# Kernel tuning notes

Measured on AMD Instinct MI355X. Metric: run time of the kernel, lower is better.

## Reference

```python
import jax, jax.numpy as jnp
import numpy as np

K = 5            # spline kernel size per dim
NUM_CLASSES = 10
EPS = 1e-4       # matches module's normalize eps
ROUTING_ITERS = 3
_BITS = jnp.array([[(b >> 2) & 1, (b >> 1) & 1, b & 1] for b in range(8)], dtype=jnp.float32)  # [8,3]


def normalize(t, axis=-1):
    return t / (jnp.sqrt(jnp.sum(t * t, axis=axis, keepdims=True)) + EPS)


def quat_mul(q, r):
    # quaternions stored (x, y, z, w) -- module sets identity as [:,:,:,3]=1
    qx, qy, qz, qw = q[..., 0], q[..., 1], q[..., 2], q[..., 3]
    rx, ry, rz, rw = r[..., 0], r[..., 1], r[..., 2], r[..., 3]
    return jnp.stack([
        qw * rx + qx * rw + qy * rz - qz * ry,
        qw * ry - qx * rz + qy * rw + qz * rx,
        qw * rz + qx * ry - qy * rx + qz * rw,
        qw * rw - qx * rx - qy * ry - qz * rz,
    ], axis=-1)


def spline_conv(x, pseudo, src, dst, W, root, bias, n_nodes):
    # degree-1 open B-spline conv, kernel 5^3, in=1, out=16
    v = pseudo * (K - 1)                                   # [E,3]
    i0 = jnp.clip(jnp.floor(v), 0, K - 2)                  # [E,3]
    frac = v - i0
    i0 = i0.astype(jnp.int32)
    idx = i0[:, None, :] + _BITS.astype(jnp.int32)[None]   # [E,8,3]
    kflat = (idx[..., 0] * K + idx[..., 1]) * K + idx[..., 2]  # [E,8]
    wb = jnp.prod(jnp.where(_BITS[None] > 0, frac[:, None, :], 1.0 - frac[:, None, :]), axis=-1)  # [E,8]
    Wg = W[kflat]                                          # [E,8,16] irregular gather (dominant traffic)
    wk = jnp.einsum('eb,ebo->eo', wb, Wg)                  # [E,16]
    msg = x[src] * wk                                      # [E,16] (in-channels = 1)
    agg = jax.ops.segment_sum(msg, dst, num_segments=n_nodes)
    deg = jax.ops.segment_sum(jnp.ones_like(dst, dtype=x.dtype), dst, num_segments=n_nodes)
    return agg / jnp.maximum(deg, 1.0)[:, None] + x @ root + bias


def caps_layer(pose, act, q):
    # pose [N,I,4], act [N,I], q [I,J,4] -> pose [N,J,4], act [N,J]
    qn = normalize(q)
    pred = normalize(quat_mul(qn[None], pose[:, :, None, :]))  # [N,I,J,4]
    b = jnp.zeros(pred.shape[:3], dtype=pose.dtype)
    for _ in range(ROUTING_ITERS):
        c = jax.nn.softmax(b, axis=2) * act[:, :, None]
        s = jnp.einsum('nij,nijq->njq', c, pred)
        v = normalize(s)
        b = b + jnp.einsum('nijq,njq->nij', pred, v)
    act_out = jax.nn.sigmoid(jnp.einsum('nij,nijq,njq->nj', c, pred, v))
    return v, act_out


def pool_by_agreement(pose, act, pos, G, start, size):
    # voxel-grid clustering + agreement-weighted quaternion averaging
    g = jnp.clip(jnp.floor((pos - start) / size), 0, G - 1).astype(jnp.int32)  # [N,3]
    vid = (g[:, 0] * G + g[:, 1]) * G + g[:, 2]
    V = G ** 3
    s = jax.ops.segment_sum(act[:, :, None] * pose, vid, num_segments=V)  # [V,J,4]
    m = normalize(s)
    agree = jnp.sum(pose * m[vid], axis=-1)                                # [N,J]
    wsum = jax.ops.segment_sum(act, vid, num_segments=V)
    cnt = jax.ops.segment_sum(jnp.ones((pose.shape[0],), pose.dtype), vid, num_segments=V)
    act_out = jax.nn.sigmoid(jax.ops.segment_sum(act * agree, vid, num_segments=V) / (wsum + EPS))
    pos_out = jax.ops.segment_sum(pos, vid, num_segments=V) / (cnt[:, None] + EPS)
    return m, act_out, pos_out


def forward(x, pos, pseudo, W_spline, root, bias, lin_w, lin_b, q0, q1, q3, q5, q6, q7, edge_index):
    N = x.shape[0]
    src, dst = edge_index[0], edge_index[1]
    h = spline_conv(x, pseudo, src, dst, W_spline, root, bias, N)   # [N,16]
    quats = jax.nn.elu(h) @ lin_w + lin_b                           # [N,4]
    pose = normalize(quats.reshape(N, 1, 4))                        # [N,1,4]
    act = x.reshape(N, 1)                                           # expand to num_caps_in=1
    pose, act = caps_layer(pose, act, q0)                           # 1 -> 6
    pose, act = caps_layer(pose, act, q1)                           # 6 -> 6
    min_pos, max_pos = pos.min(), pos.max()
    rng = max_pos + 0.001 - min_pos
    pose, act, p = pool_by_agreement(pose, act, pos, 32, min_pos, rng / 32)   # -> 32768 voxels
    pose, act = caps_layer(pose, act, q3)                           # 6 -> 8
    pose, act, p = pool_by_agreement(pose, act, p, 8, min_pos, rng / 8)       # -> 512
    pose, act = caps_layer(pose, act, q5)                           # 8 -> 12
    pose, act, p = pool_by_agreement(pose, act, p, 2, min_pos, rng / 2)       # -> 8
    pose, act = caps_layer(pose, act, q6)                           # 12 -> 14
    pose, act, p = pool_by_agreement(pose, act, p, 1, min_pos - 0.5, max_pos - min_pos + 1.0)  # -> 1
    pose, act = caps_layer(pose, act, q7)                           # 14 -> 10
    return act                                                      # [1, 10]


def setup_inputs() -> dict:
    key = jax.random.key(0)
    ks = jax.random.split(key, 16)
    N, E = 50000, 800000
    def caps_q(k, i, j):
        return jax.random.normal(k, (i, j, 4), dtype=jnp.float32)
    return {
        'x': jax.random.uniform(ks[0], (N, 1), dtype=jnp.float32),
        'pos': jax.random.uniform(ks[1], (N, 3), dtype=jnp.float32),
        'pseudo': jax.random.uniform(ks[2], (E, 3), dtype=jnp.float32),
        'W_spline': jax.random.normal(ks[3], (K ** 3, 16), dtype=jnp.float32) * 0.1,
        'root': jax.random.normal(ks[4], (1, 16), dtype=jnp.float32) * 0.1,
        'bias': jnp.zeros((16,), dtype=jnp.float32),
        'lin_w': jax.random.normal(ks[5], (16, 4), dtype=jnp.float32) * 0.25,
        'lin_b': jnp.zeros((4,), dtype=jnp.float32),
        'q0': caps_q(ks[6], 1, 6),
        'q1': caps_q(ks[7], 6, 6),
        'q3': caps_q(ks[8], 6, 8),
        'q5': caps_q(ks[9], 8, 12),
        'q6': caps_q(ks[10], 12, 14),
        'q7': caps_q(ks[11], 14, NUM_CLASSES),
        'edge_index': jax.random.randint(ks[12], (2, E), 0, N, dtype=jnp.int32),
    }


def reference(x, pos, pseudo, W_spline, root, bias, lin_w, lin_b, q0, q1, q3, q5, q6, q7, edge_index):
    return forward(x, pos, pseudo, W_spline, root, bias, lin_w, lin_b, q0, q1, q3, q5, q6, q7, edge_index)
```

## Files before the change

kernel.cpp:

```cpp
#include <hip/hip_runtime.h>
#include <math.h>

#define EPS 1e-4f

__device__ __forceinline__ float sigmoidf_(float x){ return 1.0f/(1.0f+expf(-x)); }

__device__ __forceinline__ unsigned f2u_(float f){
    unsigned u = __float_as_uint(f);
    return (u & 0x80000000u) ? ~u : (u | 0x80000000u);
}
__device__ __forceinline__ float u2f_(unsigned u){
    unsigned b = (u & 0x80000000u) ? (u & 0x7FFFFFFFu) : ~u;
    return __uint_as_float(b);
}

__global__ void minmax_kernel(const float* __restrict__ p, int n, unsigned* mm){
    float lo = INFINITY, hi = -INFINITY;
    for (int i = blockIdx.x*blockDim.x + threadIdx.x; i < n; i += gridDim.x*blockDim.x){
        float v = p[i]; lo = fminf(lo, v); hi = fmaxf(hi, v);
    }
    for (int off = 32; off > 0; off >>= 1){
        lo = fminf(lo, __shfl_down(lo, off));
        hi = fmaxf(hi, __shfl_down(hi, off));
    }
    __shared__ float slo[8], shi[8];
    int wid = threadIdx.x >> 6;
    if ((threadIdx.x & 63) == 0){ slo[wid] = lo; shi[wid] = hi; }
    __syncthreads();
    if (threadIdx.x == 0){
        int nw = blockDim.x >> 6;
        for (int w = 1; w < nw; w++){ lo = fminf(lo, slo[w]); hi = fmaxf(hi, shi[w]); }
        atomicMin(&mm[0], f2u_(lo));
        atomicMax(&mm[1], f2u_(hi));
    }
}

struct __align__(32) Rec { float fr0, fr1, fr2, xv; int base, nxt, pad0, pad1; };

__global__ void edge_pack(const int* __restrict__ ei, const float* __restrict__ pseudo,
                          const float* __restrict__ x,
                          int* __restrict__ head, Rec* __restrict__ rec, int E, int N){
    int e = blockIdx.x*blockDim.x + threadIdx.x;
    if (e >= E) return;
    float p0 = pseudo[3*e], p1 = pseudo[3*e+1], p2 = pseudo[3*e+2];
    int s = ei[e], d = ei[E + e];
    float v0 = p0*4.f, v1 = p1*4.f, v2 = p2*4.f;
    float f0 = fminf(fmaxf(floorf(v0), 0.f), 3.f);
    float f1 = fminf(fmaxf(floorf(v1), 0.f), 3.f);
    float f2 = fminf(fmaxf(floorf(v2), 0.f), 3.f);
    float4 fv = make_float4(v0 - f0, v1 - f1, v2 - f2, x[s]);
    *reinterpret_cast<float4*>(&rec[e]) = fv;
    int base = ((int)f0*5 + (int)f1)*5 + (int)f2;
    int nx = atomicExch(&head[(e & 7)*N + d], e);
    *reinterpret_cast<int2*>(&rec[e].base) = make_int2(base, nx);
}

__device__ __forceinline__ int voxel_id(const float* __restrict__ pos, int n, int G,
                                        float start, float size){
    int g[3];
    #pragma unroll
    for (int k = 0; k < 3; k++){
        float gg = floorf((pos[(size_t)n*3 + k] - start) / size);
        gg = fminf(fmaxf(gg, 0.f), (float)(G - 1));
        g[k] = (int)gg;
    }
    return (g[0]*G + g[1])*G + g[2];
}

__device__ __forceinline__ void pool_geom(const unsigned* mm, int G, int mode,
                                          float& start, float& size){
    float mn = u2f_(mm[0]), mx = u2f_(mm[1]);
    if (mode == 0){ start = mn; size = (mx + 0.001f - mn) / (float)G; }
    else          { start = mn - 0.5f; size = mx - mn + 1.0f; }
}

__global__ void elist_node(const float* __restrict__ pos, int* __restrict__ head,
                           int* __restrict__ nxt, int N, int G, int mode,
                           const unsigned* __restrict__ mm){
    int n = blockIdx.x*blockDim.x + threadIdx.x;
    if (n >= N) return;
    float start, size; pool_geom(mm, G, mode, start, size);
    int v = voxel_id(pos, n, G, start, size);
    nxt[n] = atomicExch(&head[v], n);
}

__global__ __launch_bounds__(256)
void spline_node_kernel(const float* __restrict__ x, const Rec* __restrict__ rec,
                        const int* __restrict__ head,
                        const float* __restrict__ W,
                        const float* __restrict__ root, const float* __restrict__ bias,
                        const float* __restrict__ lin_w, const float* __restrict__ lin_b,
                        float* __restrict__ pose, float* __restrict__ act, int N){
    __shared__ float Ws[125*17];
    for (int i = threadIdx.x; i < 125*16; i += blockDim.x)
        Ws[(i >> 4)*17 + (i & 15)] = W[i];
    __syncthreads();
    int t = blockIdx.x*blockDim.x + threadIdx.x;
    int n = t >> 3;
    int k = t & 7;
    if (n >= N) return;

    float agg[16];
    #pragma unroll
    for (int o = 0; o < 16; o++) agg[o] = 0.f;

    int cnt = 0;
    for (int e = head[k*N + n]; e >= 0; ){
        const Rec* rp = &rec[e];
        float4 rv = *reinterpret_cast<const float4*>(rp);
        int2  ri = *reinterpret_cast<const int2*>(&rp->base);
        e = ri.y;
        float fr0 = rv.x, fr1 = rv.y, fr2 = rv.z, xv = rv.w;
        #pragma unroll
        for (int b = 0; b < 8; b++){
            int b0 = (b >> 2) & 1, b1 = (b >> 1) & 1, b2 = b & 1;
            float w = (b0 ? fr0 : 1.f - fr0) * (b1 ? fr1 : 1.f - fr1) * (b2 ? fr2 : 1.f - fr2);
            w *= xv;
            const float* Wr = &Ws[(ri.x + b0*25 + b1*5 + b2)*17];
            #pragma unroll
            for (int o = 0; o < 16; o++) agg[o] += w * Wr[o];
        }
        cnt++;
    }

    #pragma unroll
    for (int o = 0; o < 16; o++){
        agg[o] += __shfl_xor(agg[o], 1);
        agg[o] += __shfl_xor(agg[o], 2);
        agg[o] += __shfl_xor(agg[o], 4);
    }
    cnt += __shfl_xor(cnt, 1);
    cnt += __shfl_xor(cnt, 2);
    cnt += __shfl_xor(cnt, 4);

    if (k != 0) return;

    float deg = fmaxf((float)cnt, 1.0f);
    float xs = x[n];
    float qv0 = lin_b[0], qv1 = lin_b[1], qv2 = lin_b[2], qv3 = lin_b[3];
    #pragma unroll
    for (int o = 0; o < 16; o++){
        float h = agg[o] / deg + xs * root[o] + bias[o];
        float e = (h > 0.f) ? h : expm1f(h);
        qv0 += e * lin_w[o*4 + 0];
        qv1 += e * lin_w[o*4 + 1];
        qv2 += e * lin_w[o*4 + 2];
        qv3 += e * lin_w[o*4 + 3];
    }
    float inv = 1.0f / (sqrtf(qv0*qv0 + qv1*qv1 + qv2*qv2 + qv3*qv3) + EPS);
    pose[(size_t)n*4 + 0] = qv0*inv;
    pose[(size_t)n*4 + 1] = qv1*inv;
    pose[(size_t)n*4 + 2] = qv2*inv;
    pose[(size_t)n*4 + 3] = qv3*inv;
    act[n] = xs;
}

template<int I, int J, int NPB>
__global__ __launch_bounds__(NPB*I*J)
void caps_coop_kernel(const float* __restrict__ poseIn, const float* __restrict__ actIn,
                      const float* __restrict__ q, float* __restrict__ poseOut,
                      float* __restrict__ actOut, int N){
    const int IJ = I*J;
    const int tid = threadIdx.x;
    const int nl  = tid / IJ;
    const int li  = tid - nl*IJ;
    const int i   = li / J;
    const int j   = li - i*J;
    const int node = blockIdx.x*NPB + nl;
    const bool on = (node < N);

    __shared__ float redA[NPB][I*J];
    __shared__ float redB[NPB][I*J];
    __shared__ float cp[NPB][I*J*4];
    __shared__ float vsh[NPB][J*4];

    float prx=0.f, pry=0.f, prz=0.f, prw=0.f, ai=0.f;
    if (on){
        float qx = q[li*4+0], qy = q[li*4+1], qz = q[li*4+2], qw = q[li*4+3];
        float qinv = 1.0f/(sqrtf(qx*qx+qy*qy+qz*qz+qw*qw)+EPS);
        qx*=qinv; qy*=qinv; qz*=qinv; qw*=qinv;
        const float* pp = &poseIn[((size_t)node*I + i)*4];
        float rx=pp[0], ry=pp[1], rz=pp[2], rw=pp[3];
        ai = actIn[(size_t)node*I + i];
        float tx = qw*rx + qx*rw + qy*rz - qz*ry;
        float ty = qw*ry - qx*rz + qy*rw + qz*rx;
        float tz = qw*rz + qx*ry - qy*rx + qz*rw;
        float tw = qw*rw - qx*rx - qy*ry - qz*rz;
        float pinv = 1.0f/(sqrtf(tx*tx+ty*ty+tz*tz+tw*tw)+EPS);
        prx=tx*pinv; pry=ty*pinv; prz=tz*pinv; prw=tw*pinv;
    }

    float b = 0.f, c = 0.f;
    for (int t = 0; t < 3; t++){
        redA[nl][li] = b;
        __syncthreads();
        float mb = -INFINITY;
        #pragma unroll
        for (int jj = 0; jj < J; jj++) mb = fmaxf(mb, redA[nl][i*J+jj]);
        float e = expf(b - mb);
        redB[nl][li] = e;
        __syncthreads();
        float s = 0.f;
        #pragma unroll
        for (int jj = 0; jj < J; jj++) s += redB[nl][i*J+jj];
        c = ai * e / s;
        cp[nl][li*4+0] = c*prx; cp[nl][li*4+1] = c*pry;
        cp[nl][li*4+2] = c*prz; cp[nl][li*4+3] = c*prw;
        __syncthreads();
        for (int idx = li; idx < J*4; idx += IJ){
            int jj = idx >> 2, comp = idx & 3;
            float acc = 0.f;
            #pragma unroll
            for (int ii = 0; ii < I; ii++) acc += cp[nl][(ii*J+jj)*4+comp];
            vsh[nl][idx] = acc;
        }
        __syncthreads();
        if (li < J){
            float a0=vsh[nl][li*4], a1=vsh[nl][li*4+1], a2=vsh[nl][li*4+2], a3=vsh[nl][li*4+3];
            float inv = 1.0f/(sqrtf(a0*a0+a1*a1+a2*a2+a3*a3)+EPS);
            vsh[nl][li*4]=a0*inv; vsh[nl][li*4+1]=a1*inv;
            vsh[nl][li*4+2]=a2*inv; vsh[nl][li*4+3]=a3*inv;
        }
        __syncthreads();
        if (t < 2){
            b += prx*vsh[nl][j*4] + pry*vsh[nl][j*4+1] + prz*vsh[nl][j*4+2] + prw*vsh[nl][j*4+3];
            __syncthreads();
        } else {
            redA[nl][li] = c*(prx*vsh[nl][j*4] + pry*vsh[nl][j*4+1]
                            + prz*vsh[nl][j*4+2] + prw*vsh[nl][j*4+3]);
            __syncthreads();
            if (li < J && on){
                float acc = 0.f;
                #pragma unroll
                for (int ii = 0; ii < I; ii++) acc += redA[nl][ii*J+li];
                actOut[(size_t)node*J + li] = sigmoidf_(acc);
                poseOut[((size_t)node*J+li)*4+0] = vsh[nl][li*4+0];
                poseOut[((size_t)node*J+li)*4+1] = vsh[nl][li*4+1];
                poseOut[((size_t)node*J+li)*4+2] = vsh[nl][li*4+2];
                poseOut[((size_t)node*J+li)*4+3] = vsh[nl][li*4+3];
            }
        }
    }
}

template<int J>
__global__ __launch_bounds__(256)
void pool1_gather_kernel(const float* __restrict__ pose, const float* __restrict__ act,
                         const float* __restrict__ pos,
                         const int* __restrict__ head, const int* __restrict__ nxt,
                         float* __restrict__ poseOut, float* __restrict__ actOut,
                         float* __restrict__ posOut, int V){
    int v = blockIdx.x*blockDim.x + threadIdx.x;
    if (v >= V) return;

    float s[J][4], w[J], ps0=0.f, ps1=0.f, ps2=0.f;
    #pragma unroll
    for (int j = 0; j < J; j++){ s[j][0]=0.f; s[j][1]=0.f; s[j][2]=0.f; s[j][3]=0.f; w[j]=0.f; }

    int cnt = 0;
    for (int n = head[v]; n >= 0; n = nxt[n]){
        const float* pb = &pose[(size_t)n*J*4];
        const float* ab = &act[(size_t)n*J];
        #pragma unroll
        for (int j = 0; j < J; j++){
            float aj = ab[j];
            s[j][0] += aj*pb[j*4+0];
            s[j][1] += aj*pb[j*4+1];
            s[j][2] += aj*pb[j*4+2];
            s[j][3] += aj*pb[j*4+3];
            w[j] += aj;
        }
        ps0 += pos[(size_t)n*3+0];
        ps1 += pos[(size_t)n*3+1];
        ps2 += pos[(size_t)n*3+2];
        cnt++;
    }
    #pragma unroll
    for (int j = 0; j < J; j++){
        float inv = 1.0f/(sqrtf(s[j][0]*s[j][0]+s[j][1]*s[j][1]+
                                s[j][2]*s[j][2]+s[j][3]*s[j][3])+EPS);
        s[j][0]*=inv; s[j][1]*=inv; s[j][2]*=inv; s[j][3]*=inv;
    }
    float ag[J];
    #pragma unroll
    for (int j = 0; j < J; j++) ag[j] = 0.f;
    for (int n = head[v]; n >= 0; n = nxt[n]){
        const float* pb = &pose[(size_t)n*J*4];
        const float* ab = &act[(size_t)n*J];
        #pragma unroll
        for (int j = 0; j < J; j++){
            float agree = pb[j*4+0]*s[j][0] + pb[j*4+1]*s[j][1]
                        + pb[j*4+2]*s[j][2] + pb[j*4+3]*s[j][3];
            ag[j] += ab[j]*agree;
        }
    }
    #pragma unroll
    for (int j = 0; j < J; j++){
        size_t o = (size_t)v*J + j;
        actOut[o] = sigmoidf_(ag[j] / (w[j] + EPS));
        poseOut[o*4+0] = s[j][0];
        poseOut[o*4+1] = s[j][1];
        poseOut[o*4+2] = s[j][2];
        poseOut[o*4+3] = s[j][3];
    }
    float c = (float)cnt + EPS;
    posOut[(size_t)v*3+0] = ps0 / c;
    posOut[(size_t)v*3+1] = ps1 / c;
    posOut[(size_t)v*3+2] = ps2 / c;
}

template<int V, int J, int CH, int NCHUNK>
__global__ void pool_priv1(const float4* __restrict__ poseIn, const float* __restrict__ actIn,
                           const float* __restrict__ posIn,
                           float* __restrict__ s, float* __restrict__ wsum,
                           float* __restrict__ cnt, float* __restrict__ psum,
                           int N, int G, int mode, const unsigned* __restrict__ mm){
    __shared__ float s_[V*CH*4];
    __shared__ float wsum_[V*CH];
    __shared__ float cnt_[V];
    __shared__ float psum_[V*3];
    const int chunk = blockIdx.x % NCHUNK;
    const int slice = blockIdx.x / NCHUNK;
    const int nslices = gridDim.x / NCHUNK;
    const int c0 = chunk * CH;

    for (int t = threadIdx.x; t < V*CH*4; t += blockDim.x) s_[t] = 0.f;
    for (int t = threadIdx.x; t < V*CH; t += blockDim.x) wsum_[t] = 0.f;
    if (chunk == 0){
        for (int t = threadIdx.x; t < V; t += blockDim.x) cnt_[t] = 0.f;
        for (int t = threadIdx.x; t < V*3; t += blockDim.x) psum_[t] = 0.f;
    }
    __syncthreads();

    float start, size; pool_geom(mm, G, mode, start, size);
    int per = (N + nslices - 1) / nslices;
    int n0 = slice * per, n1 = min(N, n0 + per);

    for (int n = n0 + (int)threadIdx.x; n < n1; n += blockDim.x){
        int vid = voxel_id(posIn, n, G, start, size);
        #pragma unroll
        for (int jj = 0; jj < CH; jj++){
            int j = c0 + jj;
            float aj = actIn[(size_t)n*J + j];
            float4 p = poseIn[(size_t)n*J + j];
            int b = (vid*CH + jj)*4;
            atomicAdd(&s_[b+0], aj*p.x);
            atomicAdd(&s_[b+1], aj*p.y);
            atomicAdd(&s_[b+2], aj*p.z);
            atomicAdd(&s_[b+3], aj*p.w);
            atomicAdd(&wsum_[vid*CH + jj], aj);
        }
        if (chunk == 0){
            atomicAdd(&cnt_[vid], 1.0f);
            atomicAdd(&psum_[vid*3+0], posIn[(size_t)n*3+0]);
            atomicAdd(&psum_[vid*3+1], posIn[(size_t)n*3+1]);
            atomicAdd(&psum_[vid*3+2], posIn[(size_t)n*3+2]);
        }
    }
    __syncthreads();

    for (int t = threadIdx.x; t < V*CH*4; t += blockDim.x){
        float val = s_[t];
        if (val != 0.f){
            int v = t / (CH*4), r = t % (CH*4);
            atomicAdd(&s[((size_t)v*J + c0)*4 + r], val);
        }
    }
    for (int t = threadIdx.x; t < V*CH; t += blockDim.x){
        float val = wsum_[t];
        if (val != 0.f){
            int v = t / CH, jj = t % CH;
            atomicAdd(&wsum[(size_t)v*J + c0 + jj], val);
        }
    }
    if (chunk == 0){
        for (int t = threadIdx.x; t < V; t += blockDim.x)
            if (cnt_[t] != 0.f) atomicAdd(&cnt[t], cnt_[t]);
        for (int t = threadIdx.x; t < V*3; t += blockDim.x)
            if (psum_[t] != 0.f) atomicAdd(&psum[t], psum_[t]);
    }
}

template<int V, int J>
__global__ void pool_priv2(const float4* __restrict__ poseIn, const float* __restrict__ actIn,
                           const float* __restrict__ posIn, const float4* __restrict__ m,
                           float* __restrict__ agacc,
                           int N, int G, int mode, const unsigned* __restrict__ mm){
    __shared__ float ag_[V*J];
    for (int t = threadIdx.x; t < V*J; t += blockDim.x) ag_[t] = 0.f;
    __syncthreads();
    float start, size; pool_geom(mm, G, mode, start, size);
    int nslices = gridDim.x;
    int per = (N + nslices - 1) / nslices;
    int n0 = blockIdx.x * per, n1 = min(N, n0 + per);
    for (int n = n0 + (int)threadIdx.x; n < n1; n += blockDim.x){
        int vid = voxel_id(posIn, n, G, start, size);
        #pragma unroll
        for (int j = 0; j < J; j++){
            float4 p  = poseIn[(size_t)n*J + j];
            float4 mv = m[(size_t)vid*J + j];
            float agree = p.x*mv.x + p.y*mv.y + p.z*mv.z + p.w*mv.w;
            atomicAdd(&ag_[vid*J + j], actIn[(size_t)n*J + j]*agree);
        }
    }
    __syncthreads();
    for (int t = threadIdx.x; t < V*J; t += blockDim.x)
        if (ag_[t] != 0.f) atomicAdd(&agacc[t], ag_[t]);
}

__global__ void pool_m(const float* __restrict__ s, float* __restrict__ m, int VJ){
    int t = blockIdx.x*blockDim.x + threadIdx.x;
    if (t >= VJ) return;
    float a = s[(size_t)t*4], b = s[(size_t)t*4+1], c = s[(size_t)t*4+2], d = s[(size_t)t*4+3];
    float inv = 1.0f / (sqrtf(a*a + b*b + c*c + d*d) + EPS);
    m[(size_t)t*4]   = a*inv;
    m[(size_t)t*4+1] = b*inv;
    m[(size_t)t*4+2] = c*inv;
    m[(size_t)t*4+3] = d*inv;
}

__global__ void pool_fin(const float* __restrict__ agacc, const float* __restrict__ wsum,
                         const float* __restrict__ cnt, const float* __restrict__ psum,
                         float* __restrict__ actOut, float* __restrict__ posOut, int V, int J){
    int t = blockIdx.x*blockDim.x + threadIdx.x;
    if (t >= V*J) return;
    int v = t / J, j = t % J;
    actOut[t] = sigmoidf_(agacc[t] / (wsum[t] + EPS));
    if (j == 0){
        float c = cnt[v] + EPS;
        posOut[(size_t)v*3 + 0] = psum[(size_t)v*3 + 0] / c;
        posOut[(size_t)v*3 + 1] = psum[(size_t)v*3 + 1] / c;
        posOut[(size_t)v*3 + 2] = psum[(size_t)v*3 + 2] / c;
    }
}

template<int V, int J, int CH>
__global__ void pool_fused_kernel(const float* __restrict__ poseIn, const float* __restrict__ actIn,
                                  const float* __restrict__ posIn,
                                  float* __restrict__ poseOut, float* __restrict__ actOut,
                                  float* __restrict__ posOut,
                                  int N, int G, int mode, const unsigned* __restrict__ mm){
    __shared__ float s_[V*CH*4];
    __shared__ float wsum_[V*CH];
    __shared__ float ag_[V*CH];
    __shared__ float cnt_[V];
    __shared__ float psum_[V*3];
    const int c0 = blockIdx.x * CH;

    for (int t = threadIdx.x; t < V*CH*4; t += blockDim.x) s_[t] = 0.f;
    for (int t = threadIdx.x; t < V*CH; t += blockDim.x){ wsum_[t] = 0.f; ag_[t] = 0.f; }
    if (blockIdx.x == 0){
        for (int t = threadIdx.x; t < V; t += blockDim.x) cnt_[t] = 0.f;
        for (int t = threadIdx.x; t < V*3; t += blockDim.x) psum_[t] = 0.f;
    }
    __syncthreads();

    float start, size; pool_geom(mm, G, mode, start, size);

    for (int n = threadIdx.x; n < N; n += blockDim.x){
        int vid = voxel_id(posIn, n, G, start, size);
        #pragma unroll
        for (int jj = 0; jj < CH; jj++){
            int j = c0 + jj;
            float aj = actIn[(size_t)n*J + j];
            const float* pb = &poseIn[((size_t)n*J + j)*4];
            int b = (vid*CH + jj)*4;
            atomicAdd(&s_[b+0], aj*pb[0]);
            atomicAdd(&s_[b+1], aj*pb[1]);
            atomicAdd(&s_[b+2], aj*pb[2]);
            atomicAdd(&s_[b+3], aj*pb[3]);
            atomicAdd(&wsum_[vid*CH + jj], aj);
        }
        if (blockIdx.x == 0){
            atomicAdd(&cnt_[vid], 1.0f);
            atomicAdd(&psum_[vid*3+0], posIn[(size_t)n*3+0]);
            atomicAdd(&psum_[vid*3+1], posIn[(size_t)n*3+1]);
            atomicAdd(&psum_[vid*3+2], posIn[(size_t)n*3+2]);
        }
    }
    __syncthreads();

    for (int t = threadIdx.x; t < V*CH; t += blockDim.x){
        float a = s_[t*4], b = s_[t*4+1], c = s_[t*4+2], d = s_[t*4+3];
        float inv = 1.0f / (sqrtf(a*a + b*b + c*c + d*d) + EPS);
        s_[t*4] = a*inv; s_[t*4+1] = b*inv; s_[t*4+2] = c*inv; s_[t*4+3] = d*inv;
    }
    __syncthreads();

    for (int n = threadIdx.x; n < N; n += blockDim.x){
        int vid = voxel_id(posIn, n, G, start, size);
        #pragma unroll
        for (int jj = 0; jj < CH; jj++){
            int j = c0 + jj;
            const float* pb = &poseIn[((size_t)n*J + j)*4];
            const float* mb = &s_[(vid*CH + jj)*4];
            float agree = pb[0]*mb[0] + pb[1]*mb[1] + pb[2]*mb[2] + pb[3]*mb[3];
            atomicAdd(&ag_[vid*CH + jj], actIn[(size_t)n*J + j]*agree);
        }
    }
    __syncthreads();

    for (int t = threadIdx.x; t < V*CH; t += blockDim.x){
        int v = t / CH, jj = t % CH;
        size_t o = (size_t)v*J + c0 + jj;
        actOut[o] = sigmoidf_(ag_[t] / (wsum_[t] + EPS));
        poseOut[o*4+0] = s_[t*4+0];
        poseOut[o*4+1] = s_[t*4+1];
        poseOut[o*4+2] = s_[t*4+2];
        poseOut[o*4+3] = s_[t*4+3];
    }
    if (blockIdx.x == 0){
        for (int v = threadIdx.x; v < V; v += blockDim.x){
            float c = cnt_[v] + EPS;
            posOut[(size_t)v*3+0] = psum_[(size_t)v*3+0] / c;
            posOut[(size_t)v*3+1] = psum_[(size_t)v*3+1] / c;
            posOut[(size_t)v*3+2] = psum_[(size_t)v*3+2] / c;
        }
    }
}

extern "C" void kernel_launch(void* const* d_in, const int* in_sizes, int n_in,
                              void* d_out, int out_size, void* d_ws, size_t ws_size,
                              hipStream_t stream){
    const float* x      = (const float*)d_in[0];
    const float* pos    = (const float*)d_in[1];
    const float* pseudo = (const float*)d_in[2];
    const float* Wsp    = (const float*)d_in[3];
    const float* root   = (const float*)d_in[4];
    const float* bias   = (const float*)d_in[5];
    const float* lin_w  = (const float*)d_in[6];
    const float* lin_b  = (const float*)d_in[7];
    const float* q0     = (const float*)d_in[8];
    const float* q1     = (const float*)d_in[9];
    const float* q3     = (const float*)d_in[10];
    const float* q5     = (const float*)d_in[11];
    const float* q6     = (const float*)d_in[12];
    const float* q7     = (const float*)d_in[13];
    const int*   ei     = (const int*)d_in[14];
    const int N = in_sizes[0];
    const int E = in_sizes[2] / 3;
    const int V1 = 32768;

    char* ws = (char*)d_ws;
    size_t off = 0;
    auto alloc = [&](size_t bytes)->void*{
        void* p = ws + off;
        off += (bytes + 255) & ~(size_t)255;
        return p;
    };
    unsigned* mm   = (unsigned*)alloc(8);
    int* ehead     = (int*)alloc((size_t)8*N*sizeof(int));
    Rec* erec      = (Rec*)alloc((size_t)E*sizeof(Rec));
    int* vhead     = (int*)alloc((size_t)V1*sizeof(int));
    int* vnxt      = (int*)alloc((size_t)N*sizeof(int));
    float* P0  = (float*)alloc((size_t)1250000*sizeof(float));
    float* P1  = (float*)alloc((size_t)1250000*sizeof(float));
    float* A0  = (float*)alloc((size_t)310000*sizeof(float));
    float* A1  = (float*)alloc((size_t)310000*sizeof(float));
    float* PB0 = (float*)alloc((size_t)100000*sizeof(float));
    float* PB1 = (float*)alloc((size_t)100000*sizeof(float));
    size_t pool_off0 = off;
    float* vs  = (float*)alloc((size_t)512*8*4*sizeof(float));
    float* vw  = (float*)alloc((size_t)512*8*sizeof(float));
    float* va  = (float*)alloc((size_t)512*8*sizeof(float));
    float* vc  = (float*)alloc((size_t)512*sizeof(float));
    float* vp  = (float*)alloc((size_t)512*3*sizeof(float));
    size_t pool_bytes = off - pool_off0;

    hipMemsetAsync(mm,     0xFF, 4, stream);
    hipMemsetAsync(mm + 1, 0x00, 4, stream);
    hipMemsetAsync(ehead, 0xFF, (size_t)8*N*sizeof(int), stream);
    hipMemsetAsync(vhead, 0xFF, (size_t)V1*sizeof(int), stream);

    minmax_kernel<<<80, 256, 0, stream>>>(pos, N*3, mm);

    edge_pack<<<(E + 255)/256, 256, 0, stream>>>(ei, pseudo, x, ehead, erec, E, N);
    spline_node_kernel<<<(8*N + 255)/256, 256, 0, stream>>>(x, erec, ehead, Wsp,
                                                            root, bias, lin_w, lin_b, P0, A0, N);

    caps_coop_kernel<1,6,32><<<(N + 31)/32, 32*6, 0, stream>>>(P0, A0, q0, P1, A1, N);
    caps_coop_kernel<6,6,7><<<(N + 6)/7, 7*36, 0, stream>>>(P1, A1, q1, P0, A0, N);

    {
        const int G = 32;
        elist_node<<<(N + 255)/256, 256, 0, stream>>>(pos, vhead, vnxt, N, G, 0, mm);
        pool1_gather_kernel<6><<<(V1 + 255)/256, 256, 0, stream>>>(P0, A0, pos, vhead, vnxt,
                                                                   P1, A1, PB0, V1);
    }
    caps_coop_kernel<6,8,5><<<(32768 + 4)/5, 5*48, 0, stream>>>(P1, A1, q3, P0, A0, 32768);

    {
        const int V = 512, J = 8, G = 8, NSL = 64;
        hipMemsetAsync(vs, 0, pool_bytes, stream);
        pool_priv1<V,J,4,2><<<2*NSL, 256, 0, stream>>>((const float4*)P0, A0, PB0,
                                                       vs, vw, vc, vp, 32768, G, 0, mm);
        pool_m<<<(V*J + 255)/256, 256, 0, stream>>>(vs, P1, V*J);
        pool_priv2<V,J><<<NSL, 256, 0, stream>>>((const float4*)P0, A0, PB0,
                                                 (const float4*)P1, va, 32768, G, 0, mm);
        pool_fin<<<(V*J + 255)/256, 256, 0, stream>>>(va, vw, vc, vp, A1, PB1, V, J);
    }
    caps_coop_kernel<8,12,2><<<256, 2*96, 0, stream>>>(P1, A1, q5, P0, A0, 512);

    {
        const int V = 8, J = 12, G = 2, NSL = 16;
        hipMemsetAsync(vs, 0, pool_bytes, stream);
        pool_priv1<V,J,12,1><<<NSL, 256, 0, stream>>>((const float4*)P0, A0, PB1,
                                                      vs, vw, vc, vp, 512, G, 0, mm);
        pool_m<<<1, 256, 0, stream>>>(vs, P1, V*J);
        pool_priv2<V,J><<<NSL, 256, 0, stream>>>((const float4*)P0, A0, PB1,
                                                 (const float4*)P1, va, 512, G, 0, mm);
        pool_fin<<<1, 256, 0, stream>>>(va, vw, vc, vp, A1, PB0, V, J);
    }
    caps_coop_kernel<12,14,1><<<8, 168, 0, stream>>>(P1, A1, q6, P0, A0, 8);

    pool_fused_kernel<1,14,14><<<1, 1024, 0, stream>>>(P0, A0, PB0, P1, A1, PB1, 8, 1, 1, mm);
    caps_coop_kernel<14,10,1><<<1, 140, 0, stream>>>(P1, A1, q7, P0, (float*)d_out, 1);
}
```

Measured before the change: 335.0 us.

## Replace per-destination linked edge lists with CSR via atomic rank and scan

Edges are no longer threaded into eight linked lists per destination node with atomicExch. Each edge now gets a rank from an atomicAdd on its destination's degree, a single-block scan turns degrees into offsets, and records are scattered into contiguous CSR slots. The spline kernel then reads each node's edges with strided contiguous loads instead of chasing dependent pointers, and takes the degree directly from the offsets. In exchange it adds two kernel launches, one of them a serial single-block scan over N, plus an extra rank array.

Result: slower. 434.7 us (+29.8%).

```diff
diff --git a/kernel.cpp b/kernel.cpp
--- a/kernel.cpp
+++ b/kernel.cpp
@@ -35,11 +35,42 @@
     }
 }
 
-struct __align__(32) Rec { float fr0, fr1, fr2, xv; int base, nxt, pad0, pad1; };
+
+__global__ void edge_rank(const int* __restrict__ ei, int* __restrict__ deg,
+                          int* __restrict__ rank, int E){
+    int e = blockIdx.x*blockDim.x + threadIdx.x;
+    if (e >= E) return;
+    rank[e] = atomicAdd(&deg[ei[E + e]], 1);
+}
+
+__global__ __launch_bounds__(1024)
+void deg_scan(const int* __restrict__ deg, int* __restrict__ off, int N){
+    __shared__ int part[1024];
+    const int t = threadIdx.x;
+    const int C = (N + 1023) >> 10;
+    const int base = t*C;
+    int s = 0;
+    for (int i = 0; i < C; i++){ int idx = base + i; if (idx < N) s += deg[idx]; }
+    part[t] = s;
+    __syncthreads();
+    for (int d = 1; d < 1024; d <<= 1){
+        int v = (t >= d) ? part[t - d] : 0;
+        __syncthreads();
+        part[t] += v;
+        __syncthreads();
+    }
+    int run = (t == 0) ? 0 : part[t-1];
+    for (int i = 0; i < C; i++){
+        int idx = base + i;
+        if (idx < N){ off[idx] = run; run += deg[idx]; }
+    }
+    if (t == 1023) off[N] = part[1023];
+}
 
 __global__ void edge_pack(const int* __restrict__ ei, const float* __restrict__ pseudo,
                           const float* __restrict__ x,
-                          int* __restrict__ head, Rec* __restrict__ rec, int E, int N){
+                          const int* __restrict__ rank, const int* __restrict__ off,
+                          float4* __restrict__ rec4, int* __restrict__ recb, int E){
     int e = blockIdx.x*blockDim.x + threadIdx.x;
     if (e >= E) return;
     float p0 = pseudo[3*e], p1 = pseudo[3*e+1], p2 = pseudo[3*e+2];
@@ -48,11 +79,9 @@
     float f0 = fminf(fmaxf(floorf(v0), 0.f), 3.f);
     float f1 = fminf(fmaxf(floorf(v1), 0.f), 3.f);
     float f2 = fminf(fmaxf(floorf(v2), 0.f), 3.f);
-    float4 fv = make_float4(v0 - f0, v1 - f1, v2 - f2, x[s]);
-    *reinterpret_cast<float4*>(&rec[e]) = fv;
-    int base = ((int)f0*5 + (int)f1)*5 + (int)f2;
-    int nx = atomicExch(&head[(e & 7)*N + d], e);
-    *reinterpret_cast<int2*>(&rec[e].base) = make_int2(base, nx);
+    int slot = off[d] + rank[e];
+    rec4[slot] = make_float4(v0 - f0, v1 - f1, v2 - f2, x[s]);
+    recb[slot] = ((int)f0*5 + (int)f1)*5 + (int)f2;
 }
 
 __device__ __forceinline__ int voxel_id(const float* __restrict__ pos, int n, int G,
@@ -85,8 +114,8 @@
 }
 
 __global__ __launch_bounds__(256)
-void spline_node_kernel(const float* __restrict__ x, const Rec* __restrict__ rec,
-                        const int* __restrict__ head,
+void spline_node_kernel(const float* __restrict__ x, const float4* __restrict__ rec4,
+                        const int* __restrict__ recb, const int* __restrict__ off,
                         const float* __restrict__ W,
                         const float* __restrict__ root, const float* __restrict__ bias,
                         const float* __restrict__ lin_w, const float* __restrict__ lin_b,
@@ -100,27 +129,25 @@
     int k = t & 7;
     if (n >= N) return;
 
+    int o0 = off[n], o1 = off[n+1];
+
     float agg[16];
     #pragma unroll
     for (int o = 0; o < 16; o++) agg[o] = 0.f;
 
-    int cnt = 0;
-    for (int e = head[k*N + n]; e >= 0; ){
-        const Rec* rp = &rec[e];
-        float4 rv = *reinterpret_cast<const float4*>(rp);
-        int2  ri = *reinterpret_cast<const int2*>(&rp->base);
-        e = ri.y;
+    for (int s = o0 + k; s < o1; s += 8){
+        float4 rv = rec4[s];
+        int base = recb[s];
         float fr0 = rv.x, fr1 = rv.y, fr2 = rv.z, xv = rv.w;
         #pragma unroll
         for (int b = 0; b < 8; b++){
             int b0 = (b >> 2) & 1, b1 = (b >> 1) & 1, b2 = b & 1;
             float w = (b0 ? fr0 : 1.f - fr0) * (b1 ? fr1 : 1.f - fr1) * (b2 ? fr2 : 1.f - fr2);
             w *= xv;
-            const float* Wr = &Ws[(ri.x + b0*25 + b1*5 + b2)*17];
+            const float* Wr = &Ws[(base + b0*25 + b1*5 + b2)*17];
             #pragma unroll
             for (int o = 0; o < 16; o++) agg[o] += w * Wr[o];
         }
-        cnt++;
     }
 
     #pragma unroll
@@ -129,13 +156,10 @@
         agg[o] += __shfl_xor(agg[o], 2);
         agg[o] += __shfl_xor(agg[o], 4);
     }
-    cnt += __shfl_xor(cnt, 1);
-    cnt += __shfl_xor(cnt, 2);
-    cnt += __shfl_xor(cnt, 4);
 
     if (k != 0) return;
 
-    float deg = fmaxf((float)cnt, 1.0f);
+    float deg = fmaxf((float)(o1 - o0), 1.0f);
     float xs = x[n];
     float qv0 = lin_b[0], qv1 = lin_b[1], qv2 = lin_b[2], qv3 = lin_b[3];
     #pragma unroll
@@ -549,8 +573,11 @@
         return p;
     };
     unsigned* mm   = (unsigned*)alloc(8);
-    int* ehead     = (int*)alloc((size_t)8*N*sizeof(int));
-    Rec* erec      = (Rec*)alloc((size_t)E*sizeof(Rec));
+    int* deg       = (int*)alloc((size_t)N*sizeof(int));
+    int* erank     = (int*)alloc((size_t)E*sizeof(int));
+    int* eoff      = (int*)alloc((size_t)(N+1)*sizeof(int));
+    float4* rec4   = (float4*)alloc((size_t)E*sizeof(float4));
+    int* recb      = (int*)alloc((size_t)E*sizeof(int));
     int* vhead     = (int*)alloc((size_t)V1*sizeof(int));
     int* vnxt      = (int*)alloc((size_t)N*sizeof(int));
     float* P0  = (float*)alloc((size_t)1250000*sizeof(float));
@@ -569,13 +596,15 @@
 
     hipMemsetAsync(mm,     0xFF, 4, stream);
     hipMemsetAsync(mm + 1, 0x00, 4, stream);
-    hipMemsetAsync(ehead, 0xFF, (size_t)8*N*sizeof(int), stream);
+    hipMemsetAsync(deg, 0, (size_t)N*sizeof(int), stream);
     hipMemsetAsync(vhead, 0xFF, (size_t)V1*sizeof(int), stream);
 
     minmax_kernel<<<80, 256, 0, stream>>>(pos, N*3, mm);
 
-    edge_pack<<<(E + 255)/256, 256, 0, stream>>>(ei, pseudo, x, ehead, erec, E, N);
-    spline_node_kernel<<<(8*N + 255)/256, 256, 0, stream>>>(x, erec, ehead, Wsp,
+    edge_rank<<<(E + 255)/256, 256, 0, stream>>>(ei, deg, erank, E);
+    deg_scan<<<1, 1024, 0, stream>>>(deg, eoff, N);
+    edge_pack<<<(E + 255)/256, 256, 0, stream>>>(ei, pseudo, x, erank, eoff, rec4, recb, E);
+    spline_node_kernel<<<(8*N + 255)/256, 256, 0, stream>>>(x, rec4, recb, eoff, Wsp,
                                                             root, bias, lin_w, lin_b, P0, A0, N);
 
     caps_coop_kernel<1,6,32><<<(N + 31)/32, 32*6, 0, stream>>>(P0, A0, q0, P1, A1, N);
```
